# Kernel tuning notes

Hardware: AMD Instinct MI355X
Metric: run time of the kernel (lower is better)

Reference implementation:

```python
import jax, jax.numpy as jnp
import numpy as np

A0 = 0.5291772105638411
KE = 14.399645351950548
KEHALF = KE / 2.0

def softplus_inverse(x):
    x = np.asarray(x, dtype=np.float64)
    return np.float32(x + np.log(-np.expm1(-x)))

def setup_inputs() -> dict:
    key = jax.random.key(0)
    k1, k2, k3, k4 = jax.random.split(key, 4)
    B, N, K = 16, 8192, 128
    neighbors = jax.random.randint(k1, (B, N, K), 0, N, dtype=jnp.int64)
    neighbor_mask = jnp.ones((B, N, K), dtype=jnp.float32)
    # atomic numbers in [1, 94] (Z=0 would break d/dp of Z**p)
    atomic_numbers = jax.random.randint(k2, (B, N), 0, 94, dtype=jnp.int64) + 1
    # distances scaled into a physical range [0.5, 5.5) Angstrom to avoid r->0
    distances = jax.random.uniform(k3, (B, N, K), dtype=jnp.float32) * 5.0 + 0.5
    p = lambda v: jnp.full((1,), softplus_inverse(v), dtype=jnp.float32)
    return {
        'neighbors': neighbors,
        'neighbor_mask': neighbor_mask,
        'atomic_numbers': atomic_numbers,
        'distances': distances,
        'adiv': p(1.0 / (0.8854 * A0)),
        'apow': p(0.23),
        'c1': p(0.1818), 'c2': p(0.5099), 'c3': p(0.2802), 'c4': p(0.02817),
        'a1': p(3.2), 'a2': p(0.9423), 'a3': p(0.4028), 'a4': p(0.2016),
    }

def reference(neighbors, neighbor_mask, atomic_numbers, distances,
              adiv, apow, c1, c2, c3, c4, a1, a2, a3, a4):
    sp = jax.nn.softplus
    Zf = atomic_numbers.astype(jnp.float32)            # [B, N]
    zpow = Zf ** sp(apow)                              # [B, N]
    # per-batch gather over neighbor index (sparse edge list, no NxN build)
    gather = jax.vmap(lambda v, nb: v[nb])             # ([N],[N,K]) -> [N,K]
    zpow_j = gather(zpow, neighbors)                   # [B, N, K]
    a = (zpow[:, :, None] + zpow_j) * sp(adiv) * neighbor_mask
    zizj = Zf[:, :, None] * gather(Zf, neighbors) * neighbor_mask
    c1s, c2s, c3s, c4s = sp(c1), sp(c2), sp(c3), sp(c4)
    csum = c1s + c2s + c3s + c4s
    f = (c1s / csum) * jnp.exp(-sp(a1) * a * distances) \
      + (c2s / csum) * jnp.exp(-sp(a2) * a * distances) \
      + (c3s / csum) * jnp.exp(-sp(a3) * a * distances) \
      + (c4s / csum) * jnp.exp(-sp(a4) * a * distances)
    corr = jnp.where(neighbor_mask != 0,
                     KEHALF * f * zizj / distances,
                     jnp.zeros_like(distances))        # [B, N, K]
    return jnp.sum(corr, axis=(-1, -2))[:, None]       # [B, 1]
```

## Files before the change

kernel.cpp:

```cpp
#include <hip/hip_runtime.h>


#define KEHALF_F 7.199822675975274f
#define LOG2E_F  1.4426950408889634f
#define WPB   4
#define EPI   128
#define ITERS 16

__device__ __forceinline__ float softplus_f(float x) {
    return (x > 20.f) ? x : log1pf(__expf(x));
}

__global__ void zbl_pre(const int* __restrict__ zn,
                        const float* __restrict__ adiv,
                        const float* __restrict__ apow,
                        const float* __restrict__ c1, const float* __restrict__ c2,
                        const float* __restrict__ c3, const float* __restrict__ c4,
                        const float* __restrict__ a1, const float* __restrict__ a2,
                        const float* __restrict__ a3, const float* __restrict__ a4,
                        unsigned short* __restrict__ packed, float* __restrict__ scal,
                        int total_atoms)
{
    int i = blockIdx.x * blockDim.x + threadIdx.x;
    const float spa = softplus_f(apow[0]);
    const float sad = softplus_f(adiv[0]);
    const float qb  = sad;
    const float qmax = sad * __expf(spa * __logf(94.f));
    const float qs  = (qmax - qb) * (1.f / 511.f);
    if (i == 0) {
        float s1 = softplus_f(c1[0]), s2 = softplus_f(c2[0]);
        float s3 = softplus_f(c3[0]), s4 = softplus_f(c4[0]);
        float inv = KEHALF_F / (s1 + s2 + s3 + s4);
        float w1 = s1 * inv, w2 = s2 * inv, w3 = s3 * inv, w4 = s4 * inv;
        scal[0] = sad;
        scal[1] = w1; scal[2] = w2; scal[3] = w3; scal[4] = w4;
        scal[5] = -softplus_f(a1[0]) * LOG2E_F;
        scal[6] = -softplus_f(a2[0]) * LOG2E_F;
        scal[7] = -softplus_f(a3[0]) * LOG2E_F;
        scal[8] = -softplus_f(a4[0]) * LOG2E_F;
        scal[9]  = qb;
        scal[10] = qs;
        scal[11] = __log2f(w1);
        scal[12] = __log2f(w2);
        scal[13] = __log2f(w3);
        scal[14] = __log2f(w4);
    }
    if (i < total_atoms) {
        unsigned int Z = (unsigned int)zn[i];
        float Zf = (float)Z;
        float zps = sad * __expf(spa * __logf(Zf));
        float qf = (zps - qb) / qs;
        int q = (int)(qf + 0.5f);
        if (q < 0) q = 0;
        if (q > 511) q = 511;
        packed[i] = (unsigned short)(((unsigned)q << 7) | (Z & 0x7Fu));
    }
}

extern __shared__ unsigned short tab[];

#define COMP(ii, i2, m2, d2) do {                                                 \
    const unsigned int wi_ = tab[(unsigned)(rw + (ii) * EPI) >> kshift];          \
    const unsigned int wj0 = tab[i2.x];                                           \
    const unsigned int wj1 = tab[i2.y];                                           \
    const float zpi = fmaf((float)(wi_ >> 7), qs, qb);                            \
    const float Zi  = (float)(wi_ & 0x7Fu);                                       \
    const float zpj0 = fmaf((float)(wj0 >> 7), qs, qb);                           \
    const float Zj0  = (float)(wj0 & 0x7Fu);                                      \
    const float zpj1 = fmaf((float)(wj1 >> 7), qs, qb);                           \
    const float Zj1  = (float)(wj1 & 0x7Fu);                                      \
    const float zz0 = Zi * Zj0 * m2.x;                                            \
    const float zz1 = Zi * Zj1 * m2.y;                                            \
    const float ad0 = (zpi + zpj0) * (m2.x * d2.x);                               \
    const float ad1 = (zpi + zpj1) * (m2.y * d2.y);                               \
    const float f0 = exp2f(fmaf(e1, ad0, l1)) + exp2f(fmaf(e2, ad0, l2))          \
                   + exp2f(fmaf(e3, ad0, l3)) + exp2f(fmaf(e4, ad0, l4));         \
    const float f1 = exp2f(fmaf(e1, ad1, l1)) + exp2f(fmaf(e2, ad1, l2))          \
                   + exp2f(fmaf(e3, ad1, l3)) + exp2f(fmaf(e4, ad1, l4));         \
    acc += f0 * zz0 * __builtin_amdgcn_rcpf(d2.x);                                \
    acc += f1 * zz1 * __builtin_amdgcn_rcpf(d2.y);                                \
} while (0)

#define LOAD(i2, m2, d2, ii) do {                                                 \
    i2 = *(const int2*)  (nb_ + (ii) * EPI + (lane << 1));                        \
    m2 = *(const float2*)(mk_ + (ii) * EPI + (lane << 1));                        \
    d2 = *(const float2*)(ds_ + (ii) * EPI + (lane << 1));                        \
} while (0)

__global__ __launch_bounds__(256, 8) void zbl_main13(
        const int*            __restrict__ neighbors,
        const float*          __restrict__ mask,
        const float*          __restrict__ dist,
        const unsigned short* __restrict__ packed,
        const float*          __restrict__ scal,
        float*                __restrict__ out,
        int N, int kshift, int epb)
{
    __shared__ float wsum[WPB];

    const int tid  = threadIdx.x;
    const int w    = tid >> 6;
    const int lane = tid & 63;
    const int b    = blockIdx.y;

    const int rw = (blockIdx.x * WPB + w) * (ITERS * EPI);
    const size_t ebase = (size_t)b * epb + (size_t)rw;
    const int*   nb_ = neighbors + ebase;
    const float* mk_ = mask      + ebase;
    const float* ds_ = dist      + ebase;

    const uint4* s4 = (const uint4*)(packed + (size_t)b * N);
    const int n4 = N >> 3;
    uint4 tv0, tv1, tv2, tv3;
    const bool g0 = (tid       < n4);
    const bool g1 = (tid + 256 < n4);
    const bool g2 = (tid + 512 < n4);
    const bool g3 = (tid + 768 < n4);
    if (g0) tv0 = s4[tid];
    if (g1) tv1 = s4[tid + 256];
    if (g2) tv2 = s4[tid + 512];
    if (g3) tv3 = s4[tid + 768];

    int2 iA, iB; float2 mA, dA, mB, dB;
    LOAD(iA, mA, dA, 0);
    LOAD(iB, mB, dB, 1);

    {
        uint4* t4 = (uint4*)tab;
        if (g0) t4[tid]       = tv0;
        if (g1) t4[tid + 256] = tv1;
        if (g2) t4[tid + 512] = tv2;
        if (g3) t4[tid + 768] = tv3;
    }
    const float e1 = scal[5],  e2 = scal[6],  e3 = scal[7],  e4 = scal[8];
    const float qb = scal[9],  qs = scal[10];
    const float l1 = scal[11], l2 = scal[12], l3 = scal[13], l4 = scal[14];
    __syncthreads();

    float acc = 0.f;

    int it = 0;
    for (; it < ITERS - 3; it += 2) {
        COMP(it, iA, mA, dA);
        LOAD(iA, mA, dA, it + 2);
        COMP(it + 1, iB, mB, dB);
        LOAD(iB, mB, dB, it + 3);
    }
    COMP(ITERS - 2, iA, mA, dA);
    COMP(ITERS - 1, iB, mB, dB);

    #pragma unroll
    for (int off = 32; off > 0; off >>= 1) acc += __shfl_down(acc, off);
    if (lane == 0) wsum[w] = acc;
    __syncthreads();
    if (tid == 0) {
        float t = 0.f;
        #pragma unroll
        for (int i = 0; i < WPB; ++i) t += wsum[i];
        atomicAdd(&out[b], t);
    }
}

__global__ void zbl_fallback(const int* __restrict__ neighbors,
                             const float* __restrict__ mask,
                             const float* __restrict__ dist,
                             const unsigned short* __restrict__ packed,
                             const float* __restrict__ scal,
                             float* __restrict__ out,
                             int N, int K, int epb, int total_edges)
{
    const int e = blockIdx.x * blockDim.x + threadIdx.x;
    if (e >= total_edges) return;
    const float e1 = scal[5], e2 = scal[6], e3 = scal[7], e4 = scal[8];
    const float qb = scal[9], qs = scal[10];
    const float l1 = scal[11], l2 = scal[12], l3 = scal[13], l4 = scal[14];
    const int b = e / epb;
    const int n = (e - b * epb) / K;
    const unsigned int wi = packed[(size_t)b * N + n];
    const unsigned int wj = packed[(size_t)b * N + neighbors[e]];
    const float zpi = fmaf((float)(wi >> 7), qs, qb);
    const float zpj = fmaf((float)(wj >> 7), qs, qb);
    const float Zi = (float)(wi & 0x7Fu), Zj = (float)(wj & 0x7Fu);
    const float m = mask[e], d = dist[e];
    const float ad = (zpi + zpj) * (m * d);
    const float f = exp2f(fmaf(e1, ad, l1)) + exp2f(fmaf(e2, ad, l2))
                  + exp2f(fmaf(e3, ad, l3)) + exp2f(fmaf(e4, ad, l4));
    const float corr = (m != 0.f) ? (f * Zi * Zj * m / d) : 0.f;
    if (corr != 0.f) atomicAdd(&out[b], corr);
}

extern "C" void kernel_launch(void* const* d_in, const int* in_sizes, int n_in,
                              void* d_out, int out_size, void* d_ws, size_t ws_size,
                              hipStream_t stream) {
    const int*   neighbors = (const int*)  d_in[0];
    const float* nb_mask   = (const float*)d_in[1];
    const int*   zn        = (const int*)  d_in[2];
    const float* dist      = (const float*)d_in[3];
    const float* adiv = (const float*)d_in[4];
    const float* apow = (const float*)d_in[5];
    const float* c1 = (const float*)d_in[6];
    const float* c2 = (const float*)d_in[7];
    const float* c3 = (const float*)d_in[8];
    const float* c4 = (const float*)d_in[9];
    const float* a1 = (const float*)d_in[10];
    const float* a2 = (const float*)d_in[11];
    const float* a3 = (const float*)d_in[12];
    const float* a4 = (const float*)d_in[13];

    const int total_edges = in_sizes[0];
    const int total_atoms = in_sizes[2];
    const int B = out_size;
    const int N = total_atoms / B;
    const int K = total_edges / total_atoms;
    const int epb = N * K;

    float*          scal   = (float*)d_ws;
    unsigned short* packed = (unsigned short*)((char*)d_ws + 64);

    hipMemsetAsync(d_out, 0, (size_t)out_size * sizeof(float), stream);

    {
        const int threads = 256;
        const int blocks = (total_atoms + threads - 1) / threads;
        zbl_pre<<<blocks, threads, 0, stream>>>(zn, adiv, apow, c1, c2, c3, c4,
                                                a1, a2, a3, a4,
                                                packed, scal, total_atoms);
    }

    int kshift = 0;
    while ((1 << kshift) < K && kshift < 30) kshift++;
    const bool kpow2 = ((1 << kshift) == K);

    const int span_block = WPB * EPI * ITERS;
    const bool fast = kpow2 && (kshift >= 7) && (N % 8 == 0) && (N <= 8192) &&
                      (epb % span_block == 0) &&
                      ((size_t)(64 + (size_t)total_atoms * 2) <= ws_size);
    if (fast) {
        const int bpb = epb / span_block;
        dim3 grid(bpb, B);
        zbl_main13<<<grid, 256, (size_t)N * 2, stream>>>(
            neighbors, nb_mask, dist, packed, scal, (float*)d_out,
            N, kshift, epb);
    } else {
        const int threads = 256;
        const int blocks = (total_edges + threads - 1) / threads;
        zbl_fallback<<<blocks, threads, 0, stream>>>(
            neighbors, nb_mask, dist, packed, scal, (float*)d_out,
            N, K, epb, total_edges);
    }
}
```

Measured before the change: 57.88 us.

## Stream edge data into LDS via async global_load_lds with double buffering

Replaces the register-based prefetch of neighbor, mask and distance pairs with asynchronous global-to-LDS loads (global_load_lds, 16 bytes per lane) into a per-wave two-slot staging buffer, synchronised with explicit vmcnt/lgkmcnt waits. Each lane now handles four edges per iteration instead of two, doubling the per-wave span, and launch bounds drop from 8 to 4 blocks per SM. The aim is deeper memory-latency hiding and wider loads without spending registers. In exchange it uses about 24KB of extra LDS per block, which may cut occupancy, and relies on hand-written waitcnt ordering for correctness.

```diff
diff --git a/kernel.cpp b/kernel.cpp
--- a/kernel.cpp
+++ b/kernel.cpp
@@ -3,9 +3,11 @@
 
 #define KEHALF_F 7.199822675975274f
 #define LOG2E_F  1.4426950408889634f
-#define WPB   4
-#define EPI   128
-#define ITERS 16
+#define DEPTH    2
+#define GRAN     256
+#define WPB      4
+#define SLOTB    3072
+#define ITERS    16
 
 __device__ __forceinline__ float softplus_f(float x) {
     return (x > 20.f) ? x : log1pf(__expf(x));
@@ -59,35 +61,57 @@
 
 extern __shared__ unsigned short tab[];
 
-#define COMP(ii, i2, m2, d2) do {                                                 \
-    const unsigned int wi_ = tab[(unsigned)(rw + (ii) * EPI) >> kshift];          \
-    const unsigned int wj0 = tab[i2.x];                                           \
-    const unsigned int wj1 = tab[i2.y];                                           \
+#define STAGE3(slotp, it) do {                                                    \
+    const char* _gi = (const char*)(nb_ + ((it) << 8)) + lane * 16;               \
+    const char* _gm = (const char*)(mk_ + ((it) << 8)) + lane * 16;               \
+    const char* _gd = (const char*)(ds_ + ((it) << 8)) + lane * 16;               \
+    __builtin_amdgcn_global_load_lds(                                             \
+        (const __attribute__((address_space(1))) void*)_gi,                       \
+        (__attribute__((address_space(3))) void*)(slotp), 16, 0, 0);              \
+    __builtin_amdgcn_global_load_lds(                                             \
+        (const __attribute__((address_space(1))) void*)_gm,                       \
+        (__attribute__((address_space(3))) void*)((slotp) + 1024), 16, 0, 0);     \
+    __builtin_amdgcn_global_load_lds(                                             \
+        (const __attribute__((address_space(1))) void*)_gd,                       \
+        (__attribute__((address_space(3))) void*)((slotp) + 2048), 16, 0, 0);     \
+} while (0)
+
+#define BODY(it) do {                                                             \
+    char* sp = &stage[w][(it) & (DEPTH - 1)][0];                                  \
+    const int4   j4 = *(const int4*)  (sp + (lane << 4));                         \
+    const float4 m4 = *(const float4*)(sp + 1024 + (lane << 4));                  \
+    const float4 d4 = *(const float4*)(sp + 2048 + (lane << 4));                  \
+    const int r = rw + ((it) << 8) + (lane << 2);                                 \
+    const unsigned int wi_ = tab[(unsigned)r >> kshift];                          \
+    const unsigned int wj0 = tab[j4.x];                                           \
+    const unsigned int wj1 = tab[j4.y];                                           \
+    const unsigned int wj2 = tab[j4.z];                                           \
+    const unsigned int wj3 = tab[j4.w];                                           \
     const float zpi = fmaf((float)(wi_ >> 7), qs, qb);                            \
     const float Zi  = (float)(wi_ & 0x7Fu);                                       \
-    const float zpj0 = fmaf((float)(wj0 >> 7), qs, qb);                           \
-    const float Zj0  = (float)(wj0 & 0x7Fu);                                      \
-    const float zpj1 = fmaf((float)(wj1 >> 7), qs, qb);                           \
-    const float Zj1  = (float)(wj1 & 0x7Fu);                                      \
-    const float zz0 = Zi * Zj0 * m2.x;                                            \
-    const float zz1 = Zi * Zj1 * m2.y;                                            \
-    const float ad0 = (zpi + zpj0) * (m2.x * d2.x);                               \
-    const float ad1 = (zpi + zpj1) * (m2.y * d2.y);                               \
+    const float zpj0 = fmaf((float)(wj0 >> 7), qs, qb), Zj0 = (float)(wj0 & 0x7Fu);\
+    const float zpj1 = fmaf((float)(wj1 >> 7), qs, qb), Zj1 = (float)(wj1 & 0x7Fu);\
+    const float zpj2 = fmaf((float)(wj2 >> 7), qs, qb), Zj2 = (float)(wj2 & 0x7Fu);\
+    const float zpj3 = fmaf((float)(wj3 >> 7), qs, qb), Zj3 = (float)(wj3 & 0x7Fu);\
+    const float ad0 = (zpi + zpj0) * (m4.x * d4.x);                               \
+    const float ad1 = (zpi + zpj1) * (m4.y * d4.y);                               \
+    const float ad2 = (zpi + zpj2) * (m4.z * d4.z);                               \
+    const float ad3 = (zpi + zpj3) * (m4.w * d4.w);                               \
     const float f0 = exp2f(fmaf(e1, ad0, l1)) + exp2f(fmaf(e2, ad0, l2))          \
                    + exp2f(fmaf(e3, ad0, l3)) + exp2f(fmaf(e4, ad0, l4));         \
     const float f1 = exp2f(fmaf(e1, ad1, l1)) + exp2f(fmaf(e2, ad1, l2))          \
                    + exp2f(fmaf(e3, ad1, l3)) + exp2f(fmaf(e4, ad1, l4));         \
-    acc += f0 * zz0 * __builtin_amdgcn_rcpf(d2.x);                                \
-    acc += f1 * zz1 * __builtin_amdgcn_rcpf(d2.y);                                \
+    const float f2 = exp2f(fmaf(e1, ad2, l1)) + exp2f(fmaf(e2, ad2, l2))          \
+                   + exp2f(fmaf(e3, ad2, l3)) + exp2f(fmaf(e4, ad2, l4));         \
+    const float f3 = exp2f(fmaf(e1, ad3, l1)) + exp2f(fmaf(e2, ad3, l2))          \
+                   + exp2f(fmaf(e3, ad3, l3)) + exp2f(fmaf(e4, ad3, l4));         \
+    acc += f0 * (Zi * Zj0 * m4.x) * __builtin_amdgcn_rcpf(d4.x);                  \
+    acc += f1 * (Zi * Zj1 * m4.y) * __builtin_amdgcn_rcpf(d4.y);                  \
+    acc += f2 * (Zi * Zj2 * m4.z) * __builtin_amdgcn_rcpf(d4.z);                  \
+    acc += f3 * (Zi * Zj3 * m4.w) * __builtin_amdgcn_rcpf(d4.w);                  \
 } while (0)
 
-#define LOAD(i2, m2, d2, ii) do {                                                 \
-    i2 = *(const int2*)  (nb_ + (ii) * EPI + (lane << 1));                        \
-    m2 = *(const float2*)(mk_ + (ii) * EPI + (lane << 1));                        \
-    d2 = *(const float2*)(ds_ + (ii) * EPI + (lane << 1));                        \
-} while (0)
-
-__global__ __launch_bounds__(256, 8) void zbl_main13(
+__global__ __launch_bounds__(256, 4) void zbl_main14(
         const int*            __restrict__ neighbors,
         const float*          __restrict__ mask,
         const float*          __restrict__ dist,
@@ -96,14 +120,14 @@
         float*                __restrict__ out,
         int N, int kshift, int epb)
 {
-    __shared__ float wsum[WPB];
+    __shared__ char stage[WPB][DEPTH][SLOTB];
 
     const int tid  = threadIdx.x;
     const int w    = tid >> 6;
     const int lane = tid & 63;
     const int b    = blockIdx.y;
 
-    const int rw = (blockIdx.x * WPB + w) * (ITERS * EPI);
+    const int rw = (blockIdx.x * WPB + w) * (ITERS * GRAN);
     const size_t ebase = (size_t)b * epb + (size_t)rw;
     const int*   nb_ = neighbors + ebase;
     const float* mk_ = mask      + ebase;
@@ -121,9 +145,10 @@
     if (g2) tv2 = s4[tid + 512];
     if (g3) tv3 = s4[tid + 768];
 
-    int2 iA, iB; float2 mA, dA, mB, dB;
-    LOAD(iA, mA, dA, 0);
-    LOAD(iB, mB, dB, 1);
+    {
+        char* sp0 = &stage[w][0][0]; STAGE3(sp0, 0);
+        char* sp1 = &stage[w][1][0]; STAGE3(sp1, 1);
+    }
 
     {
         uint4* t4 = (uint4*)tab;
@@ -138,25 +163,61 @@
     __syncthreads();
 
     float acc = 0.f;
-
     int it = 0;
-    for (; it < ITERS - 3; it += 2) {
-        COMP(it, iA, mA, dA);
-        LOAD(iA, mA, dA, it + 2);
-        COMP(it + 1, iB, mB, dB);
-        LOAD(iB, mB, dB, it + 3);
-    }
-    COMP(ITERS - 2, iA, mA, dA);
-    COMP(ITERS - 1, iB, mB, dB);
+
+    for (; it <= ITERS - 3; ++it) {
+        asm volatile("s_waitcnt vmcnt(3)" ::: "memory");
+        char* sp = &stage[w][it & (DEPTH - 1)][0];
+        const int4   j4 = *(const int4*)  (sp + (lane << 4));
+        const float4 m4 = *(const float4*)(sp + 1024 + (lane << 4));
+        const float4 d4 = *(const float4*)(sp + 2048 + (lane << 4));
+        asm volatile("s_waitcnt lgkmcnt(0)" ::: "memory");
+        STAGE3(sp, it + 2);
+        const int r = rw + (it << 8) + (lane << 2);
+        const unsigned int wi_ = tab[(unsigned)r >> kshift];
+        const unsigned int wj0 = tab[j4.x];
+        const unsigned int wj1 = tab[j4.y];
+        const unsigned int wj2 = tab[j4.z];
+        const unsigned int wj3 = tab[j4.w];
+        const float zpi = fmaf((float)(wi_ >> 7), qs, qb);
+        const float Zi  = (float)(wi_ & 0x7Fu);
+        const float zpj0 = fmaf((float)(wj0 >> 7), qs, qb), Zj0 = (float)(wj0 & 0x7Fu);
+        const float zpj1 = fmaf((float)(wj1 >> 7), qs, qb), Zj1 = (float)(wj1 & 0x7Fu);
+        const float zpj2 = fmaf((float)(wj2 >> 7), qs, qb), Zj2 = (float)(wj2 & 0x7Fu);
+        const float zpj3 = fmaf((float)(wj3 >> 7), qs, qb), Zj3 = (float)(wj3 & 0x7Fu);
+        const float ad0 = (zpi + zpj0) * (m4.x * d4.x);
+        const float ad1 = (zpi + zpj1) * (m4.y * d4.y);
+        const float ad2 = (zpi + zpj2) * (m4.z * d4.z);
+        const float ad3 = (zpi + zpj3) * (m4.w * d4.w);
+        const float f0 = exp2f(fmaf(e1, ad0, l1)) + exp2f(fmaf(e2, ad0, l2))
+                       + exp2f(fmaf(e3, ad0, l3)) + exp2f(fmaf(e4, ad0, l4));
+        const float f1 = exp2f(fmaf(e1, ad1, l1)) + exp2f(fmaf(e2, ad1, l2))
+                       + exp2f(fmaf(e3, ad1, l3)) + exp2f(fmaf(e4, ad1, l4));
+        const float f2 = exp2f(fmaf(e1, ad2, l1)) + exp2f(fmaf(e2, ad2, l2))
+                       + exp2f(fmaf(e3, ad2, l3)) + exp2f(fmaf(e4, ad2, l4));
+        const float f3 = exp2f(fmaf(e1, ad3, l1)) + exp2f(fmaf(e2, ad3, l2))
+                       + exp2f(fmaf(e3, ad3, l3)) + exp2f(fmaf(e4, ad3, l4));
+        acc += f0 * (Zi * Zj0 * m4.x) * __builtin_amdgcn_rcpf(d4.x);
+        acc += f1 * (Zi * Zj1 * m4.y) * __builtin_amdgcn_rcpf(d4.y);
+        acc += f2 * (Zi * Zj2 * m4.z) * __builtin_amdgcn_rcpf(d4.z);
+        acc += f3 * (Zi * Zj3 * m4.w) * __builtin_amdgcn_rcpf(d4.w);
+    }
+
+    asm volatile("s_waitcnt vmcnt(3)" ::: "memory");
+    BODY(ITERS - 2); ++it;
+    asm volatile("s_waitcnt vmcnt(0)" ::: "memory");
+    BODY(ITERS - 1);
 
     #pragma unroll
     for (int off = 32; off > 0; off >>= 1) acc += __shfl_down(acc, off);
-    if (lane == 0) wsum[w] = acc;
+    __syncthreads();
+    float* wred = (float*)&stage[0][0][0];
+    if (lane == 0) wred[w] = acc;
     __syncthreads();
     if (tid == 0) {
         float t = 0.f;
         #pragma unroll
-        for (int i = 0; i < WPB; ++i) t += wsum[i];
+        for (int i = 0; i < WPB; ++i) t += wred[i];
         atomicAdd(&out[b], t);
     }
 }
@@ -231,14 +292,14 @@
     while ((1 << kshift) < K && kshift < 30) kshift++;
     const bool kpow2 = ((1 << kshift) == K);
 
-    const int span_block = WPB * EPI * ITERS;
-    const bool fast = kpow2 && (kshift >= 7) && (N % 8 == 0) && (N <= 8192) &&
+    const int span_block = WPB * GRAN * ITERS;
+    const bool fast = kpow2 && (kshift >= 2) && (N % 8 == 0) && (N <= 8192) &&
                       (epb % span_block == 0) &&
                       ((size_t)(64 + (size_t)total_atoms * 2) <= ws_size);
     if (fast) {
         const int bpb = epb / span_block;
         dim3 grid(bpb, B);
-        zbl_main13<<<grid, 256, (size_t)N * 2, stream>>>(
+        zbl_main14<<<grid, 256, (size_t)N * 2, stream>>>(
             neighbors, nb_mask, dist, packed, scal, (float*)d_out,
             N, kshift, epb);
     } else {
```

New measurement: 55.77 us. 1.04x faster.
